# Kernel optimization log

Measured on AMD Instinct MI355X. Metric: run time of the kernel, lower is better.

## Reference

```python
import jax, jax.numpy as jnp
import numpy as np

L, B, S, H, V = 6, 8, 2048, 768, 32000
FF = 4 * H
EPS = 1e-5


def _ln(x, g, b):
    m = x.mean(-1, keepdims=True)
    v = ((x - m) ** 2).mean(-1, keepdims=True)
    return (x - m) / jnp.sqrt(v + EPS) * g + b


def setup_inputs() -> dict:
    key = jax.random.key(0)
    ks = iter(jax.random.split(key, 32))
    std = 0.02
    n = lambda shape: jax.random.normal(next(ks), shape, dtype=jnp.float32) * std
    inp = {
        'input_ids': jax.random.randint(next(ks), (B, S), 0, V, dtype=jnp.int64),
        'attention_mask': jnp.ones((B, S), dtype=jnp.int32),
        'tok_emb': n((V, H)),
        'pos_emb': n((S, H)),
        'Wq': n((L, H, H)), 'bq': n((L, H)),
        'Wk': n((L, H, H)), 'bk': n((L, H)),
        'Wv': n((L, H, H)), 'bv': n((L, H)),
        'Wo': n((L, H, H)), 'bo': n((L, H)),
        'ln1_g': jnp.ones((L, H), jnp.float32), 'ln1_b': jnp.zeros((L, H), jnp.float32),
        'ln2_g': jnp.ones((L, H), jnp.float32), 'ln2_b': jnp.zeros((L, H), jnp.float32),
        'W1': n((L, H, FF)), 'b1': n((L, FF)),
        'W2': n((L, FF, H)), 'b2': n((L, H)),
        'fln_g': jnp.ones((H,), jnp.float32), 'fln_b': jnp.zeros((H,), jnp.float32),
        'cls_W': n((H, 1)), 'cls_b': n((1,)),
    }
    return inp


def reference(input_ids, attention_mask, tok_emb, pos_emb, Wq, bq, Wk, bk, Wv, bv,
              Wo, bo, ln1_g, ln1_b, ln2_g, ln2_b, W1, b1, W2, b2,
              fln_g, fln_b, cls_W, cls_b):
    x = tok_emb[input_ids] + pos_emb[None, :S, :]  # [B,S,H]
    causal = jnp.triu(jnp.ones((S, S), dtype=bool), 1)  # True above diagonal
    pad = ~(attention_mask.astype(bool))[:, None, :]    # [B,1,S] True where padded
    full_mask = causal[None, :, :] | pad                # [B,S,S]
    scale = 1.0 / (H ** 0.5)
    for i in range(L):
        # --- attention block (pre-LN) ---
        h = _ln(x, ln1_g[i], ln1_b[i])
        q = h @ Wq[i] + bq[i]
        k = h @ Wk[i] + bk[i]
        v = h @ Wv[i] + bv[i]
        scores = jnp.einsum('bqd,bkd->bqk', q, k) * scale
        scores = jnp.where(full_mask, -jnp.inf, scores)
        attn = jax.nn.softmax(scores, axis=-1)
        o = jnp.einsum('bqk,bkd->bqd', attn, v) @ Wo[i] + bo[i]
        x = o + x
        # --- FFN block ---
        h = _ln(x, ln2_g[i], ln2_b[i])
        x = jax.nn.gelu(h @ W1[i] + b1[i], approximate=False) @ W2[i] + b2[i] + x
    x = _ln(x, fln_g, fln_b)
    # select hidden state of last non-padded token per row
    m = attention_mask.astype(jnp.int32)
    last = m.sum(1) - 1                      # [B]
    x_last = x[jnp.arange(B), last]          # [B,H]
    logits = x_last @ cls_W + cls_b          # [B,1]
    return logits
```

## Files before the change

### kernel.cpp

```cpp
#include <hip/hip_runtime.h>
#include <hip/hip_bf16.h>

#define Bn 8
#define Sn 2048
#define Hn 768
#define FFn 3072
#define Ln 6
#define BSn (Bn * Sn)
#define CQ 512
#define LN_EPS 1e-5f

typedef __hip_bfloat16 bf16;
typedef __bf16 bf16x8 __attribute__((ext_vector_type(8)));
typedef float f32x4 __attribute__((ext_vector_type(4)));

__device__ __forceinline__ float b2f(bf16 v) { return __bfloat162float(v); }
__device__ __forceinline__ void stc(float* p, float v) { *p = v; }
__device__ __forceinline__ void stc(bf16* p, float v) { *p = __float2bfloat16(v); }

union Pk8 { float4 v; bf16 h[8]; };

__device__ __forceinline__ void gld16(const bf16* g, short* l) {
  __builtin_amdgcn_global_load_lds(
      (const __attribute__((address_space(1))) unsigned int*)g,
      (__attribute__((address_space(3))) unsigned int*)l, 16, 0, 0);
}

#define BAR() __builtin_amdgcn_s_barrier()
#define LGKM0()                                            \
  {                                                        \
    asm volatile("s_waitcnt lgkmcnt(0)" ::: "memory");     \
    __builtin_amdgcn_sched_barrier(0);                     \
  }
#define VMC(n) asm volatile("s_waitcnt vmcnt(" #n ")" ::: "memory")

__device__ __forceinline__ float gelu_exact(float v) {
  float a = fabsf(v) * 0.70710678118654752f;
  float t = 1.0f / (1.0f + 0.3275911f * a);
  float poly = t * (0.254829592f +
               t * (-0.284496736f +
               t * (1.421413741f +
               t * (-1.453152027f + t * 1.061405429f))));
  float er = 1.0f - poly * __expf(-a * a);
  er = v < 0.f ? -er : er;
  return 0.5f * v * (1.0f + er);
}

__global__ void __launch_bounds__(256) embed_kernel(
    const int* __restrict__ ids, const float* __restrict__ tok,
    const float* __restrict__ pos, float* __restrict__ x) {
  long t = blockIdx.x;
  int s = (int)(t & (Sn - 1));
  long id = ids[t];
  const float* tr = tok + id * Hn;
  const float* pr = pos + (long)s * Hn;
  float* xr = x + t * Hn;
  for (int d = threadIdx.x; d < Hn; d += 256)
    xr[d] = tr[d] + pr[d];
}

__global__ void __launch_bounds__(256) transpose_all_kernel(
    const float* __restrict__ Wq_l, const float* __restrict__ Wk_l,
    const float* __restrict__ Wv_l, const float* __restrict__ Wo_l,
    const float* __restrict__ W1_l, const float* __restrict__ W2_l,
    bf16* __restrict__ wt) {
  int id = blockIdx.x;
  const float* W;
  bf16* Wt;
  int K, N, tile, tilesX;
  if (id < 2304) {
    int w = id / 576;
    tile = id - w * 576;
    W = (w == 0) ? Wq_l : (w == 1) ? Wk_l : (w == 2) ? Wv_l : Wo_l;
    Wt = wt + (size_t)w * Hn * Hn;
    K = Hn; N = Hn; tilesX = Hn / 32;
  } else if (id < 4608) {
    tile = id - 2304;
    W = W1_l;
    Wt = wt + 4 * (size_t)Hn * Hn;
    K = Hn; N = FFn; tilesX = FFn / 32;
  } else {
    tile = id - 4608;
    W = W2_l;
    Wt = wt + 4 * (size_t)Hn * Hn + (size_t)Hn * FFn;
    K = FFn; N = Hn; tilesX = Hn / 32;
  }
  int n0 = (tile % tilesX) * 32, k0 = (tile / tilesX) * 32;

  __shared__ float t[32][33];
  int tx = threadIdx.x & 31, ty = threadIdx.x >> 5;
#pragma unroll
  for (int i = 0; i < 32; i += 8)
    t[ty + i][tx] = W[(long)(k0 + ty + i) * N + n0 + tx];
  __syncthreads();
#pragma unroll
  for (int i = 0; i < 32; i += 8)
    stc(Wt + (long)(n0 + ty + i) * K + k0 + tx, t[tx][ty + i]);
}

__global__ void __launch_bounds__(256) ln_kernel(
    const float* __restrict__ x, const float* __restrict__ g,
    const float* __restrict__ b, bf16* __restrict__ out) {
  long token = blockIdx.x;
  const float* xr = x + token * Hn;
  bf16* orow = out + token * Hn;
  int tid = threadIdx.x;

  float vals[3];
  float s1 = 0.f;
#pragma unroll
  for (int i = 0; i < 3; i++) {
    vals[i] = xr[tid + 256 * i];
    s1 += vals[i];
  }
  __shared__ float sb[4];
  __shared__ float stat[2];
#pragma unroll
  for (int off = 32; off > 0; off >>= 1) s1 += __shfl_down(s1, off, 64);
  if ((tid & 63) == 0) sb[tid >> 6] = s1;
  __syncthreads();
  if (tid == 0) stat[0] = (sb[0] + sb[1] + sb[2] + sb[3]) * (1.0f / Hn);
  __syncthreads();
  float mean = stat[0];

  float s2 = 0.f;
#pragma unroll
  for (int i = 0; i < 3; i++) {
    float d = vals[i] - mean;
    s2 += d * d;
  }
#pragma unroll
  for (int off = 32; off > 0; off >>= 1) s2 += __shfl_down(s2, off, 64);
  if ((tid & 63) == 0) sb[tid >> 6] = s2;
  __syncthreads();
  if (tid == 0)
    stat[1] = rsqrtf((sb[0] + sb[1] + sb[2] + sb[3]) * (1.0f / Hn) + LN_EPS);
  __syncthreads();
  float inv = stat[1];

#pragma unroll
  for (int i = 0; i < 3; i++) {
    int d = tid + 256 * i;
    stc(orow + d, (vals[i] - mean) * inv * g[d] + b[d]);
  }
}

template <int EPI, typename CT>
__global__ void __launch_bounds__(512) gemm256_kernel(
    const bf16* __restrict__ A, const bf16* __restrict__ Bt,
    const float* __restrict__ bias, const float* __restrict__ res,
    CT* __restrict__ C, int M, int N, int K,
    const float* __restrict__ bias2, const float* __restrict__ bias3) {
  __shared__ short lds[65536];
  int tid = threadIdx.x;
  int wave = tid >> 6, lane = tid & 63;
  int wm = wave >> 2, wn = wave & 3;
  int quad = lane >> 4, l16 = lane & 15;
  int swz = (l16 & 7) << 4;
  int g = lane >> 3;
  int kswz = ((lane & 7) ^ g) * 8;

  int nwg = gridDim.x, orig = blockIdx.x;
  int q8 = nwg >> 3, r8 = nwg & 7;
  int xcd = orig & 7, loc = orig >> 3;
  int wg = (xcd < r8 ? xcd * (q8 + 1) : r8 * (q8 + 1) + (xcd - r8) * q8) + loc;
  int gx = N >> 8;
  long colBase = (long)(wg % gx) * 256;
  long rowBase = (long)(wg / gx) * 256;

  const bf16* aSrc = A + rowBase * K + (long)g * K + kswz;
  const bf16* bSrc = Bt + colBase * K + (long)g * K + kswz;

  int r0A[2][2], r0B[2][2], sA[2][2], sB[2][2];
#pragma unroll
  for (int o = 0; o < 2; o++)
#pragma unroll
    for (int j = 0; j < 2; j++) {
      int c = wave * 2 + j;
      r0A[o][j] = o * 64 + ((c >> 3) << 7) + ((c & 7) << 3);
      r0B[o][j] = o * 32 + ((c >> 2) << 6) + ((c & 3) << 3);
      sA[o][j] = r0A[o][j] * K;
      sB[o][j] = r0B[o][j] * K;
    }

  char* lb = (char*)lds;
  const char* aRd0 = lb + (wm * 128 + l16) * 128 + ((quad * 16) ^ swz);
  const char* aRd1 = lb + (wm * 128 + l16) * 128 + ((64 + quad * 16) ^ swz);
  const char* bRd0 = lb + 65536 + (wn * 64 + l16) * 128 + ((quad * 16) ^ swz);
  const char* bRd1 = lb + 65536 + (wn * 64 + l16) * 128 + ((64 + quad * 16) ^ swz);

  f32x4 acc[8][4] = {};
  bf16x8 af[4][2], bfr[2][2][2];

#define STAGEA(ODD, BUF, KOFF)                                              \
  {                                                                         \
    gld16(aSrc + sA[ODD][0] + (KOFF),                                       \
          (short*)(lb + (BUF) * 32768 + r0A[ODD][0] * 128));                \
    gld16(aSrc + sA[ODD][1] + (KOFF),                                       \
          (short*)(lb + (BUF) * 32768 + r0A[ODD][1] * 128));                \
  }
#define STAGEB(ODD, BUF, KOFF)                                              \
  {                                                                         \
    gld16(bSrc + sB[ODD][0] + (KOFF),                                       \
          (short*)(lb + 65536 + (BUF) * 32768 + r0B[ODD][0] * 128));        \
    gld16(bSrc + sB[ODD][1] + (KOFF),                                       \
          (short*)(lb + 65536 + (BUF) * 32768 + r0B[ODD][1] * 128));        \
  }
#define LOADA(BUF, H)                                                       \
  {                                                                         \
    _Pragma("unroll") for (int i_ = 0; i_ < 4; i_++) {                      \
      af[i_][0] = *(const bf16x8*)(aRd0 + (BUF) * 32768 +                   \
                                   ((H) * 64 + i_ * 16) * 128);             \
      af[i_][1] = *(const bf16x8*)(aRd1 + (BUF) * 32768 +                   \
                                   ((H) * 64 + i_ * 16) * 128);             \
    }                                                                       \
  }
#define LOADB(BUF, NH)                                                      \
  {                                                                         \
    _Pragma("unroll") for (int j_ = 0; j_ < 2; j_++) {                      \
      bfr[NH][j_][0] = *(const bf16x8*)(bRd0 + (BUF) * 32768 +              \
                                        ((NH) * 32 + j_ * 16) * 128);       \
      bfr[NH][j_][1] = *(const bf16x8*)(bRd1 + (BUF) * 32768 +              \
                                        ((NH) * 32 + j_ * 16) * 128);       \
    }                                                                       \
  }
#define MFMA_PH(h, nh)                                                      \
  __builtin_amdgcn_s_setprio(1);                                            \
  _Pragma("unroll") for (int i_ = 0; i_ < 4; i_++)                          \
      _Pragma("unroll") for (int j_ = 0; j_ < 2; j_++)                      \
          _Pragma("unroll") for (int s_ = 0; s_ < 2; s_++)                  \
              acc[(h) * 4 + i_][(nh) * 2 + j_] =                            \
                  __builtin_amdgcn_mfma_f32_16x16x32_bf16(                  \
                      af[i_][s_], bfr[nh][j_][s_],                          \
                      acc[(h) * 4 + i_][(nh) * 2 + j_], 0, 0, 0);           \
  __builtin_amdgcn_s_setprio(0);

  int NT = K >> 6;
  STAGEA(0, 0, 0); STAGEB(0, 0, 0); STAGEB(1, 0, 0); STAGEA(1, 0, 0);
  STAGEA(0, 1, 64); STAGEB(0, 1, 64); STAGEB(1, 1, 64);
  VMC(6);
  BAR();

  int pairs = (NT - 2) >> 1;
  for (int p = 0; p < pairs; p++) {
    LOADA(0, 0); LOADB(0, 0); STAGEA(1, 1, 64);
    BAR(); LGKM0(); MFMA_PH(0, 0); BAR();
    LOADB(0, 1); STAGEA(0, 0, 128);
    BAR(); LGKM0(); MFMA_PH(0, 1); BAR();
    LOADA(0, 1); STAGEB(0, 0, 128);
    BAR(); LGKM0(); MFMA_PH(1, 1); BAR();
    STAGEB(1, 0, 128); VMC(6);
    BAR(); MFMA_PH(1, 0); BAR();
    LOADA(1, 0); LOADB(1, 0); STAGEA(1, 0, 128);
    BAR(); LGKM0(); MFMA_PH(0, 0); BAR();
    LOADB(1, 1); STAGEA(0, 1, 192);
    BAR(); LGKM0(); MFMA_PH(0, 1); BAR();
    LOADA(1, 1); STAGEB(0, 1, 192);
    BAR(); LGKM0(); MFMA_PH(1, 1); BAR();
    STAGEB(1, 1, 192); VMC(6);
    BAR(); MFMA_PH(1, 0); BAR();
    aSrc += 128; bSrc += 128;
  }
  LOADA(0, 0); LOADB(0, 0); STAGEA(1, 1, 64);
  BAR(); LGKM0(); MFMA_PH(0, 0); BAR();
  LOADB(0, 1);
  BAR(); LGKM0(); MFMA_PH(0, 1); BAR();
  LOADA(0, 1);
  BAR(); LGKM0(); MFMA_PH(1, 1); BAR();
  VMC(0);
  BAR(); MFMA_PH(1, 0); BAR();
  LOADA(1, 0); LOADB(1, 0);
  BAR(); LGKM0(); MFMA_PH(0, 0); BAR();
  LOADB(1, 1);
  BAR(); LGKM0(); MFMA_PH(0, 1); BAR();
  LOADA(1, 1);
  BAR(); LGKM0(); MFMA_PH(1, 1); BAR();
  BAR(); MFMA_PH(1, 0); BAR();

#pragma unroll
  for (int mi = 0; mi < 8; mi++) {
#pragma unroll
    for (int nj = 0; nj < 4; nj++) {
      int col = (int)colBase + wn * 64 + nj * 16 + l16;
      long row0 = rowBase + wm * 128 + mi * 16 + quad * 4;
      if (EPI == 4) {
        if (col < 1536) {
          float bv = col < 768 ? bias[col] : bias2[col - 768];
          bf16* dst = (bf16*)C + (col < 768 ? 0 : (size_t)BSn * Hn - Hn);
#pragma unroll
          for (int r = 0; r < 4; r++)
            stc(dst + (row0 + r) * Hn + col, acc[mi][nj][r] + bv);
        } else {
          int vcol = col - 1536;
          float bv = bias3[vcol];
          union { uint2 w; bf16 h[4]; } pk;
          long bb = row0 >> 11;
          long s = row0 & (Sn - 1);
#pragma unroll
          for (int r = 0; r < 4; r++)
            pk.h[r] = __float2bfloat16(acc[mi][nj][r] + bv);
          bf16* vT = (bf16*)C + 2 * (size_t)BSn * Hn;
          *reinterpret_cast<uint2*>(vT + (bb * Hn + vcol) * Sn + s) = pk.w;
        }
      } else {
        float bv = bias[col];
#pragma unroll
        for (int r = 0; r < 4; r++) {
          long row = row0 + r;
          float v = acc[mi][nj][r] + bv;
          if (EPI == 1) v += res[row * N + col];
          if (EPI == 2) v = gelu_exact(v);
          stc(C + row * N + col, v);
        }
      }
    }
  }
#undef STAGEA
#undef STAGEB
#undef LOADA
#undef LOADB
#undef MFMA_PH
}

__global__ void __launch_bounds__(256) qk_mfma_kernel(
    const bf16* __restrict__ q, const bf16* __restrict__ k,
    bf16* __restrict__ sc, int q0) {
  int kBase = blockIdx.x * 128;
  int qBase = q0 + blockIdx.y * 128;
  if (kBase > qBase + 127) return;
  int b = blockIdx.z;
  const bf16* Ag = q + ((long)b * Sn + qBase) * Hn;
  const bf16* Bg = k + ((long)b * Sn + kBase) * Hn;

  __shared__ short As[128 * 32];
  __shared__ short Bs[128 * 32];
  int tid = threadIdx.x;
  int wave = tid >> 6, lane = tid & 63;
  int waveM = wave >> 1, waveN = wave & 1;
  int quad = lane >> 4, l16 = lane & 15;
  int srow = lane >> 2;
  int schunk = (lane & 3) * 8;

  f32x4 acc[4][4] = {};

  for (int kt = 0; kt < Hn; kt += 32) {
#pragma unroll
    for (int c = 0; c < 2; c++) {
      int r0 = wave * 32 + c * 16;
      gld16(Ag + (long)(r0 + srow) * Hn + kt + schunk, &As[r0 * 32]);
      gld16(Bg + (long)(r0 + srow) * Hn + kt + schunk, &Bs[r0 * 32]);
    }
    __syncthreads();

    bf16x8 af[4], bfrg[4];
#pragma unroll
    for (int t = 0; t < 4; t++)
      af[t] = *(const bf16x8*)&As[(waveM * 64 + t * 16 + l16) * 32 + quad * 8];
#pragma unroll
    for (int u = 0; u < 4; u++)
      bfrg[u] = *(const bf16x8*)&Bs[(waveN * 64 + u * 16 + l16) * 32 + quad * 8];
#pragma unroll
    for (int t = 0; t < 4; t++)
#pragma unroll
      for (int u = 0; u < 4; u++)
        acc[t][u] = __builtin_amdgcn_mfma_f32_16x16x32_bf16(af[t], bfrg[u],
                                                            acc[t][u], 0, 0, 0);
    __syncthreads();
  }

  const float scale = 0.03608439182435161f;
#pragma unroll
  for (int t = 0; t < 4; t++)
#pragma unroll
    for (int u = 0; u < 4; u++) {
      int col = kBase + waveN * 64 + u * 16 + l16;
#pragma unroll
      for (int r = 0; r < 4; r++) {
        long qRel = (long)(qBase - q0) + waveM * 64 + t * 16 + quad * 4 + r;
        stc(sc + ((long)b * CQ + qRel) * Sn + col, acc[t][u][r] * scale);
      }
    }
}

__global__ void __launch_bounds__(256) pv_mfma_kernel(
    const bf16* __restrict__ p, const bf16* __restrict__ vT,
    bf16* __restrict__ o, int q0) {
  int colBase = blockIdx.x * 128;
  int qBase = q0 + blockIdx.y * 128;
  int b = blockIdx.z;
  int klimit = qBase + 128;
  const bf16* Ag = p + ((long)b * CQ + (qBase - q0)) * Sn;
  const bf16* Bg = vT + ((long)b * Hn + colBase) * Sn;

  __shared__ short As[128 * 32];
  __shared__ short Bs[128 * 32];
  int tid = threadIdx.x;
  int wave = tid >> 6, lane = tid & 63;
  int waveM = wave >> 1, waveN = wave & 1;
  int quad = lane >> 4, l16 = lane & 15;
  int srow = lane >> 2;
  int schunk = (lane & 3) * 8;

  f32x4 acc[4][4] = {};

  for (int kt = 0; kt < klimit; kt += 32) {
#pragma unroll
    for (int c = 0; c < 2; c++) {
      int r0 = wave * 32 + c * 16;
      gld16(Ag + (long)(r0 + srow) * Sn + kt + schunk, &As[r0 * 32]);
      gld16(Bg + (long)(r0 + srow) * Sn + kt + schunk, &Bs[r0 * 32]);
    }
    __syncthreads();

    bf16x8 af[4], bfrg[4];
#pragma unroll
    for (int t = 0; t < 4; t++)
      af[t] = *(const bf16x8*)&As[(waveM * 64 + t * 16 + l16) * 32 + quad * 8];
#pragma unroll
    for (int u = 0; u < 4; u++)
      bfrg[u] = *(const bf16x8*)&Bs[(waveN * 64 + u * 16 + l16) * 32 + quad * 8];
#pragma unroll
    for (int t = 0; t < 4; t++)
#pragma unroll
      for (int u = 0; u < 4; u++)
        acc[t][u] = __builtin_amdgcn_mfma_f32_16x16x32_bf16(af[t], bfrg[u],
                                                            acc[t][u], 0, 0, 0);
    __syncthreads();
  }

#pragma unroll
  for (int t = 0; t < 4; t++)
#pragma unroll
    for (int u = 0; u < 4; u++) {
      int col = colBase + waveN * 64 + u * 16 + l16;
#pragma unroll
      for (int r = 0; r < 4; r++) {
        long qAbs = (long)qBase + waveM * 64 + t * 16 + quad * 4 + r;
        stc(o + ((long)b * Sn + qAbs) * Hn + col, acc[t][u][r]);
      }
    }
}

__global__ void __launch_bounds__(256) softmax_kernel(
    bf16* __restrict__ sc, const int* __restrict__ mask, int q0) {
  int qRel = blockIdx.x;
  int b = blockIdx.y;
  int qg = q0 + qRel;
  bf16* row = sc + ((long)b * CQ + qRel) * Sn;
  const int* mrow = mask + b * Sn;
  int tid = threadIdx.x;
  int n = qg + 1;
  int limit = (qg & ~127) + 128;
  int k0 = tid * 8;

  Pk8 pk;
  pk.v = *reinterpret_cast<const float4*>(row + k0);
  int4 m0 = *reinterpret_cast<const int4*>(mrow + k0);
  int4 m1 = *reinterpret_cast<const int4*>(mrow + k0 + 4);
  int mm[8] = {m0.x, m0.y, m0.z, m0.w, m1.x, m1.y, m1.z, m1.w};

  float sv[8];
  float lmax = -1e30f;
#pragma unroll
  for (int j = 0; j < 8; j++) {
    int kk = k0 + j;
    float s = (kk < n && mm[j] != 0) ? b2f(pk.h[j]) : -1e30f;
    sv[j] = s;
    lmax = fmaxf(lmax, s);
  }
  __shared__ float sb[4];
  __shared__ float stat;
#pragma unroll
  for (int off = 32; off > 0; off >>= 1)
    lmax = fmaxf(lmax, __shfl_down(lmax, off, 64));
  if ((tid & 63) == 0) sb[tid >> 6] = lmax;
  __syncthreads();
  if (tid == 0) stat = fmaxf(fmaxf(sb[0], sb[1]), fmaxf(sb[2], sb[3]));
  __syncthreads();
  float gmax = stat;

  float ev[8];
  float lsum = 0.f;
#pragma unroll
  for (int j = 0; j < 8; j++) {
    float e = (sv[j] > -1e29f) ? __expf(sv[j] - gmax) : 0.f;
    ev[j] = e;
    lsum += e;
  }
#pragma unroll
  for (int off = 32; off > 0; off >>= 1) lsum += __shfl_down(lsum, off, 64);
  if ((tid & 63) == 0) sb[tid >> 6] = lsum;
  __syncthreads();
  if (tid == 0) stat = sb[0] + sb[1] + sb[2] + sb[3];
  __syncthreads();
  float inv = 1.0f / stat;

  if (k0 < limit) {
    Pk8 o;
#pragma unroll
    for (int j = 0; j < 8; j++)
      o.h[j] = __float2bfloat16((k0 + j < n) ? ev[j] * inv : 0.f);
    *reinterpret_cast<float4*>(row + k0) = o.v;
  }
}

__global__ void __launch_bounds__(256) cls_kernel(
    const bf16* __restrict__ h, const int* __restrict__ mask,
    const float* __restrict__ clsW, const float* __restrict__ clsb,
    float* __restrict__ out) {
  int b = blockIdx.x;
  int tid = threadIdx.x;
  __shared__ float sb[4];
  __shared__ int ib[4];
  __shared__ int lastsh;

  int ls = 0;
  for (int s = tid; s < Sn; s += 256) ls += mask[b * Sn + s];
#pragma unroll
  for (int off = 32; off > 0; off >>= 1) ls += __shfl_down(ls, off, 64);
  if ((tid & 63) == 0) ib[tid >> 6] = ls;
  __syncthreads();
  if (tid == 0) lastsh = ib[0] + ib[1] + ib[2] + ib[3] - 1;
  __syncthreads();
  int last = lastsh;

  const bf16* row = h + ((long)b * Sn + last) * Hn;
  float acc = 0.f;
  for (int d = tid; d < Hn; d += 256) acc += b2f(row[d]) * clsW[d];
#pragma unroll
  for (int off = 32; off > 0; off >>= 1) acc += __shfl_down(acc, off, 64);
  if ((tid & 63) == 0) sb[tid >> 6] = acc;
  __syncthreads();
  if (tid == 0) out[b] = sb[0] + sb[1] + sb[2] + sb[3] + clsb[0];
}

extern "C" void kernel_launch(void* const* d_in, const int* in_sizes, int n_in,
                              void* d_out, int out_size, void* d_ws,
                              size_t ws_size, hipStream_t stream) {
  const int* ids     = (const int*)d_in[0];
  const int* mask    = (const int*)d_in[1];
  const float* tok   = (const float*)d_in[2];
  const float* pos   = (const float*)d_in[3];
  const float* Wq    = (const float*)d_in[4];
  const float* bq    = (const float*)d_in[5];
  const float* Wk    = (const float*)d_in[6];
  const float* bk    = (const float*)d_in[7];
  const float* Wv    = (const float*)d_in[8];
  const float* bv    = (const float*)d_in[9];
  const float* Wo    = (const float*)d_in[10];
  const float* bo    = (const float*)d_in[11];
  const float* ln1g  = (const float*)d_in[12];
  const float* ln1b  = (const float*)d_in[13];
  const float* ln2g  = (const float*)d_in[14];
  const float* ln2b  = (const float*)d_in[15];
  const float* W1    = (const float*)d_in[16];
  const float* b1    = (const float*)d_in[17];
  const float* W2    = (const float*)d_in[18];
  const float* b2    = (const float*)d_in[19];
  const float* flng  = (const float*)d_in[20];
  const float* flnb  = (const float*)d_in[21];
  const float* clsW  = (const float*)d_in[22];
  const float* clsb  = (const float*)d_in[23];

  float* x = (float*)d_ws;
  bf16* h  = (bf16*)(x + (size_t)BSn * Hn);
  bf16* cb = h + (size_t)BSn * Hn;
  bf16* qb = cb;
  bf16* kb = cb + (size_t)BSn * Hn;
  bf16* vtb = cb + 2 * (size_t)BSn * Hn;
  bf16* scb = cb + 3 * (size_t)BSn * Hn;
  bf16* wt = cb + (size_t)BSn * FFn;
  bf16* wqT = wt;
  bf16* woT = wqT + 3 * (size_t)Hn * Hn;
  bf16* w1T = woT + (size_t)Hn * Hn;
  bf16* w2T = w1T + (size_t)Hn * FFn;

  const int M = BSn;
  dim3 blk(256);
  dim3 blk512(512);
  dim3 gridQK(Sn / 128, CQ / 128, Bn);
  dim3 gridSM(CQ, Bn);
  dim3 gridPV(Hn / 128, CQ / 128, Bn);

  embed_kernel<<<BSn, blk, 0, stream>>>(ids, tok, pos, x);

  for (int l = 0; l < Ln; l++) {
    const float* Wq_l = Wq + (size_t)l * Hn * Hn;
    const float* Wk_l = Wk + (size_t)l * Hn * Hn;
    const float* Wv_l = Wv + (size_t)l * Hn * Hn;
    const float* Wo_l = Wo + (size_t)l * Hn * Hn;
    const float* W1_l = W1 + (size_t)l * Hn * FFn;
    const float* W2_l = W2 + (size_t)l * FFn * Hn;

    transpose_all_kernel<<<6912, blk, 0, stream>>>(Wq_l, Wk_l, Wv_l, Wo_l,
                                                   W1_l, W2_l, wt);

    ln_kernel<<<BSn, blk, 0, stream>>>(x, ln1g + l * Hn, ln1b + l * Hn, h);
    gemm256_kernel<4, bf16><<<576, blk512, 0, stream>>>(
        h, wqT, bq + l * Hn, nullptr, qb, M, 3 * Hn, Hn,
        bk + l * Hn, bv + l * Hn);
    for (int c = 0; c < Sn / CQ; c++) {
      int q0 = c * CQ;
      qk_mfma_kernel<<<gridQK, blk, 0, stream>>>(qb, kb, scb, q0);
      softmax_kernel<<<gridSM, blk, 0, stream>>>(scb, mask, q0);
      pv_mfma_kernel<<<gridPV, blk, 0, stream>>>(scb, vtb, h, q0);
    }
    gemm256_kernel<1, float><<<192, blk512, 0, stream>>>(
        h, woT, bo + l * Hn, x, x, M, Hn, Hn, nullptr, nullptr);

    ln_kernel<<<BSn, blk, 0, stream>>>(x, ln2g + l * Hn, ln2b + l * Hn, h);
    gemm256_kernel<2, bf16><<<768, blk512, 0, stream>>>(
        h, w1T, b1 + l * FFn, nullptr, cb, M, FFn, Hn, nullptr, nullptr);
    gemm256_kernel<1, float><<<192, blk512, 0, stream>>>(
        cb, w2T, b2 + l * Hn, x, x, M, Hn, FFn, nullptr, nullptr);
  }

  ln_kernel<<<BSn, blk, 0, stream>>>(x, flng, flnb, h);
  cls_kernel<<<Bn, blk, 0, stream>>>(h, mask, clsW, clsb, (float*)d_out);
}
```

Baseline: 3.925 ms.

## Simplify GEMM main loop to coarse double-buffered stage/compute schedule

Replaces the hand-interleaved 8-phase GEMM loop, which had fine-grained barriers, lgkmcnt waits and partial vmcnt waits, with a simple double-buffered loop. Each iteration stages a whole K-tile into one buffer while computing from the other, then does a full vmcnt(0) wait and one barrier per tile. This cuts barrier count and lets the compiler schedule LDS reads freely. In exchange it loses the fine-grained overlap of global loads with MFMA phases and relies on compiler-inserted waits for the LDS reads.

```diff
diff --git a/kernel.cpp b/kernel.cpp
--- a/kernel.cpp
+++ b/kernel.cpp
@@ -27,11 +27,6 @@
 }
 
 #define BAR() __builtin_amdgcn_s_barrier()
-#define LGKM0()                                            \
-  {                                                        \
-    asm volatile("s_waitcnt lgkmcnt(0)" ::: "memory");     \
-    __builtin_amdgcn_sched_barrier(0);                     \
-  }
 #define VMC(n) asm volatile("s_waitcnt vmcnt(" #n ")" ::: "memory")
 
 __device__ __forceinline__ float gelu_exact(float v) {
@@ -206,6 +201,11 @@
     gld16(bSrc + sB[ODD][1] + (KOFF),                                       \
           (short*)(lb + 65536 + (BUF) * 32768 + r0B[ODD][1] * 128));        \
   }
+#define STAGE_ALL(BUF, KOFF)                                                \
+  {                                                                         \
+    STAGEA(0, BUF, KOFF); STAGEB(0, BUF, KOFF);                             \
+    STAGEA(1, BUF, KOFF); STAGEB(1, BUF, KOFF);                             \
+  }
 #define LOADA(BUF, H)                                                       \
   {                                                                         \
     _Pragma("unroll") for (int i_ = 0; i_ < 4; i_++) {                      \
@@ -234,48 +234,27 @@
                       af[i_][s_], bfr[nh][j_][s_],                          \
                       acc[(h) * 4 + i_][(nh) * 2 + j_], 0, 0, 0);           \
   __builtin_amdgcn_s_setprio(0);
+#define COMPUTE(BUF)                                                        \
+  {                                                                         \
+    LOADB(BUF, 0); LOADB(BUF, 1); LOADA(BUF, 0);                            \
+    MFMA_PH(0, 0); MFMA_PH(0, 1);                                           \
+    LOADA(BUF, 1);                                                          \
+    MFMA_PH(1, 1); MFMA_PH(1, 0);                                           \
+  }
 
   int NT = K >> 6;
-  STAGEA(0, 0, 0); STAGEB(0, 0, 0); STAGEB(1, 0, 0); STAGEA(1, 0, 0);
-  STAGEA(0, 1, 64); STAGEB(0, 1, 64); STAGEB(1, 1, 64);
-  VMC(6);
-  BAR();
-
-  int pairs = (NT - 2) >> 1;
-  for (int p = 0; p < pairs; p++) {
-    LOADA(0, 0); LOADB(0, 0); STAGEA(1, 1, 64);
-    BAR(); LGKM0(); MFMA_PH(0, 0); BAR();
-    LOADB(0, 1); STAGEA(0, 0, 128);
-    BAR(); LGKM0(); MFMA_PH(0, 1); BAR();
-    LOADA(0, 1); STAGEB(0, 0, 128);
-    BAR(); LGKM0(); MFMA_PH(1, 1); BAR();
-    STAGEB(1, 0, 128); VMC(6);
-    BAR(); MFMA_PH(1, 0); BAR();
-    LOADA(1, 0); LOADB(1, 0); STAGEA(1, 0, 128);
-    BAR(); LGKM0(); MFMA_PH(0, 0); BAR();
-    LOADB(1, 1); STAGEA(0, 1, 192);
-    BAR(); LGKM0(); MFMA_PH(0, 1); BAR();
-    LOADA(1, 1); STAGEB(0, 1, 192);
-    BAR(); LGKM0(); MFMA_PH(1, 1); BAR();
-    STAGEB(1, 1, 192); VMC(6);
-    BAR(); MFMA_PH(1, 0); BAR();
+  STAGE_ALL(0, 0);
+  VMC(0); BAR();
+
+  for (int T = 0; T < NT; T += 2) {
+    STAGE_ALL(1, 64);
+    COMPUTE(0);
+    VMC(0); BAR();
+    if (T + 2 < NT) STAGE_ALL(0, 128);
+    COMPUTE(1);
+    VMC(0); BAR();
     aSrc += 128; bSrc += 128;
   }
-  LOADA(0, 0); LOADB(0, 0); STAGEA(1, 1, 64);
-  BAR(); LGKM0(); MFMA_PH(0, 0); BAR();
-  LOADB(0, 1);
-  BAR(); LGKM0(); MFMA_PH(0, 1); BAR();
-  LOADA(0, 1);
-  BAR(); LGKM0(); MFMA_PH(1, 1); BAR();
-  VMC(0);
-  BAR(); MFMA_PH(1, 0); BAR();
-  LOADA(1, 0); LOADB(1, 0);
-  BAR(); LGKM0(); MFMA_PH(0, 0); BAR();
-  LOADB(1, 1);
-  BAR(); LGKM0(); MFMA_PH(0, 1); BAR();
-  LOADA(1, 1);
-  BAR(); LGKM0(); MFMA_PH(1, 1); BAR();
-  BAR(); MFMA_PH(1, 0); BAR();
 
 #pragma unroll
   for (int mi = 0; mi < 8; mi++) {
@@ -317,9 +296,11 @@
   }
 #undef STAGEA
 #undef STAGEB
+#undef STAGE_ALL
 #undef LOADA
 #undef LOADB
 #undef MFMA_PH
+#undef COMPUTE
 }
 
 __global__ void __launch_bounds__(256) qk_mfma_kernel(
```

After: 3.806 ms. 3.0% less time.
